# Optimization experiments

Measured on AMD Instinct MI355X. Metric: run time of the kernel, lower is better.

Reference implementation:

```python
import jax, jax.numpy as jnp
import numpy as np

SEQ_LEN = 2048
N_FFT = 4096   # rfft length n >= seq_len (repo uses next power of two of ~2*seq)
K = 24         # num_eigh
D = 768        # n_embd
BATCH = 1


def _spectral_filters(seq_len: int, k: int) -> jnp.ndarray:
    # Hankel matrix Z[i,j] = 2 / ((i+j)^3 - (i+j)), 1-indexed
    e = np.arange(1, seq_len + 1, dtype=np.float64)
    ipj = e[:, None] + e[None, :]
    Z = 2.0 / (ipj ** 3 - ipj)
    sigma, phi = np.linalg.eigh(Z)
    sigma, phi = sigma[-k:], phi[:, -k:]
    phi = phi * sigma ** 0.25
    return jnp.asarray(phi, dtype=jnp.float32)  # (seq_len, K)


def setup_inputs() -> dict:
    key = jax.random.key(0)
    k1, k2, k3 = jax.random.split(key, 3)
    x = jax.random.normal(k1, (BATCH, SEQ_LEN, D), dtype=jnp.float32)
    M_phi_plus = jax.random.normal(k2, (K, D, D), dtype=jnp.float32) * 0.02
    M_phi_minus = jax.random.normal(k3, (K, D, D), dtype=jnp.float32) * 0.02
    phi = _spectral_filters(SEQ_LEN, K)
    return {"x": x, "phi": phi, "M_phi_plus": M_phi_plus, "M_phi_minus": M_phi_minus}


def _convolve(u, v, n):
    # u: (b, seq, d), v: (seq, K)
    bsz, seq, d = u.shape
    k = v.shape[1]
    # alternating sign sequence (+1, -1, +1, ...)
    sgn = jnp.where(jnp.arange(seq) % 2 == 1, -1.0, 1.0)[None, :, None, None]  # (1,seq,1,1)
    V = jnp.fft.rfft(v.reshape(1, seq, k, 1, 1).astype(jnp.float32), n=n, axis=1)
    u4 = jnp.broadcast_to(u[:, :, None, :], (bsz, seq, k, d))  # (b,seq,K,d)
    U = jnp.stack([u4, u4 * sgn], axis=-1).astype(jnp.float32)  # (b,seq,K,d,2)
    Uf = jnp.fft.rfft(U, n=n, axis=1)
    U_conv = jnp.fft.irfft(V * Uf, n=n, axis=1)[:, :seq]  # (b,seq,K,d,2)
    U_plus = U_conv[..., 0]
    U_minus = U_conv[..., 1] * sgn
    return U_plus, U_minus


def reference(x, phi, M_phi_plus, M_phi_minus):
    U_plus, U_minus = _convolve(x, phi, N_FFT)
    spectral_plus = jnp.einsum('bskd,kde->bse', U_plus, M_phi_plus)
    spectral_minus = jnp.einsum('bskd,kde->bse', U_minus, M_phi_minus)
    return spectral_plus + spectral_minus
```

## Files before the change

### kernel.cpp

```cpp
#include <hip/hip_runtime.h>
#include <hip/hip_bf16.h>
#include <stdint.h>

#define SEQ 2048
#define DDIM 768
#define KF 24
#define NKV 48
#define NZC 8

typedef unsigned short ushort_t;
typedef __attribute__((ext_vector_type(8))) short short8;
typedef __attribute__((ext_vector_type(4))) float f32x4;

typedef __attribute__((address_space(3))) uint32_t lds_u32;
typedef __attribute__((address_space(1))) uint32_t glb_u32;

__device__ __forceinline__ unsigned short f2bf(float f) {
    union { float f; uint32_t u; } v; v.f = f;
    uint32_t u = v.u;
    return (unsigned short)((u + 0x7fff + ((u >> 16) & 1)) >> 16);
}


__global__ void k_pack_x(const float* __restrict__ x, ushort_t* __restrict__ xpk) {
    int b = blockIdx.x;
    int tt = b / 12, ks = b % 12;
    int tid = threadIdx.x;
    ushort_t* dst = xpk + (size_t)b * 8192;
    const float* src = x + (size_t)tt * 128 * DDIM + ks * 64;
#pragma unroll
    for (int p = 0; p < 4; ++p) {
        int s = p * 256 + tid;
        int row = s >> 3, sl = s & 7;
        const float* rp = src + (size_t)row * DDIM + sl * 8;
        float4 a = *(const float4*)rp;
        float4 c = *(const float4*)(rp + 4);
        ushort_t v[8] = {f2bf(a.x), f2bf(a.y), f2bf(a.z), f2bf(a.w),
                         f2bf(c.x), f2bf(c.y), f2bf(c.z), f2bf(c.w)};
        *(uint4*)(dst + row * 64 + ((sl ^ (row & 7)) << 3)) = *(uint4*)v;
    }
}

__global__ void k_pack_M(const float* __restrict__ Mp, const float* __restrict__ Mm,
                         ushort_t* __restrict__ Mpk) {
    __shared__ ushort_t lt[128 * 66];
    int b = blockIdx.x;
    int kv = b / 72; int rem = b % 72; int et = rem / 12, ks = rem % 12;
    const float* src = ((kv < KF) ? Mp + (size_t)kv * DDIM * DDIM
                                  : Mm + (size_t)(kv - KF) * DDIM * DDIM)
                       + (size_t)(ks * 64) * DDIM + et * 128;
    int tid = threadIdx.x;
#pragma unroll
    for (int p = 0; p < 32; ++p) {
        int lin = p * 256 + tid;
        int d = lin >> 7, e = lin & 127;
        lt[e * 66 + d] = f2bf(src[(size_t)d * DDIM + e]);
    }
    __syncthreads();
    ushort_t* dst = Mpk + (size_t)b * 8192;
#pragma unroll
    for (int p = 0; p < 4; ++p) {
        int s = p * 256 + tid; int row = s >> 3, sl = s & 7;
        ushort_t v[8];
#pragma unroll
        for (int j = 0; j < 8; ++j) v[j] = lt[row * 66 + sl * 8 + j];
        *(uint4*)(dst + row * 64 + ((sl ^ (row & 7)) << 3)) = *(uint4*)v;
    }
}

__global__ void k_build_T(const float* __restrict__ phi, ushort_t* __restrict__ Tpk) {
    __shared__ float phiL[256];
    int b = blockIdx.x;
    int kv = b / 17, slot = b % 17;
    int dm = slot - 1;
    int k = kv % KF; bool neg = kv >= KF;
    int tid = threadIdx.x;
    int tau = 128 * dm - 127 + tid;
    float v = 0.f;
    if (tid < 255 && tau >= 0 && tau < SEQ) {
        v = phi[(size_t)tau * KF + k];
        if (neg && (tau & 1)) v = -v;
    }
    phiL[tid] = v;
    __syncthreads();
    ushort_t* dst = Tpk + (size_t)b * 2 * 8192;
#pragma unroll
    for (int h = 0; h < 2; ++h) {
#pragma unroll
        for (int p = 0; p < 4; ++p) {
            int s = p * 256 + tid; int row = s >> 3, sl = s & 7;
            ushort_t v8[8];
#pragma unroll
            for (int j = 0; j < 8; ++j) {
                int col = h * 64 + sl * 8 + j;
                v8[j] = f2bf(phiL[row - col + 127]);
            }
            *(uint4*)(dst + h * 8192 + row * 64 + ((sl ^ (row & 7)) << 3)) = *(uint4*)v8;
        }
    }
}


__device__ __forceinline__ void read_frags(const ushort_t* As, const ushort_t* Bs,
                                           int lane, int wm, int wn, int kk,
                                           short8 av[4], short8 bv[4]) {
    int slot = kk * 4 + (lane >> 4);
#pragma unroll
    for (int m = 0; m < 4; ++m) {
        int row = wm * 64 + m * 16 + (lane & 15);
        av[m] = *(const short8*)(As + row * 64 + ((slot ^ (row & 7)) << 3));
    }
#pragma unroll
    for (int n = 0; n < 4; ++n) {
        int row = wn * 64 + n * 16 + (lane & 15);
        bv[n] = *(const short8*)(Bs + row * 64 + ((slot ^ (row & 7)) << 3));
    }
}

__device__ __forceinline__ void mfma16(const short8 av[4], const short8 bv[4], f32x4 acc[4][4]) {
    __builtin_amdgcn_s_setprio(1);
#pragma unroll
    for (int m = 0; m < 4; ++m)
#pragma unroll
        for (int n = 0; n < 4; ++n)
            acc[m][n] = __builtin_amdgcn_mfma_f32_16x16x32_bf16(av[m], bv[n], acc[m][n], 0, 0, 0);
    __builtin_amdgcn_s_setprio(0);
}

__global__ __launch_bounds__(256, 2)
void k_gemm_A(const ushort_t* __restrict__ Mpk, const ushort_t* __restrict__ xpk,
              ushort_t* __restrict__ Apk) {
    __shared__ ushort_t smem[2][2][8192];
    int bid = blockIdx.x;
    int lid = (bid & 7) * 576 + (bid >> 3);
    int kv = lid / 96; int rem = lid % 96; int et = rem / 16, tt = rem % 16;
    const ushort_t* Abase = Mpk + ((size_t)(kv * 6 + et) * 12) * 8192;
    const ushort_t* Bbase = xpk + (size_t)(tt * 12) * 8192;
    int tid = threadIdx.x, lane = tid & 63, wave = tid >> 6;
    int wm = wave >> 1, wn = wave & 1;

    auto stage4 = [&](const ushort_t* src, ushort_t* dst) {
        const char* s = (const char*)src + wave * 4096 + lane * 16;
        char* l = (char*)dst + wave * 4096;
#pragma unroll
        for (int p = 0; p < 4; ++p)
            __builtin_amdgcn_global_load_lds((const glb_u32*)(s + p * 1024),
                                             (lds_u32*)(l + p * 1024), 16, 0, 0);
    };

    f32x4 acc[4][4];
#pragma unroll
    for (int m = 0; m < 4; ++m)
#pragma unroll
        for (int n = 0; n < 4; ++n) acc[m][n] = (f32x4){0.f, 0.f, 0.f, 0.f};

    stage4(Abase, smem[0][0]);
    stage4(Bbase, smem[0][1]);

    for (int s = 0; s < 12; ++s) {
        int c = s & 1;
        bool more = (s + 1 < 12);
        if (more) {
            stage4(Abase + (s + 1) * 8192, smem[c ^ 1][0]);
            asm volatile("s_waitcnt vmcnt(4)" ::: "memory");
        } else {
            asm volatile("s_waitcnt vmcnt(0)" ::: "memory");
        }
        __builtin_amdgcn_s_barrier();
        __builtin_amdgcn_sched_barrier(0);

        const ushort_t* As = smem[c][0];
        const ushort_t* Bs = smem[c][1];
        short8 av[2][4], bv[2][4];
#pragma unroll
        for (int kk = 0; kk < 2; ++kk) {
            int slot = kk * 4 + (lane >> 4);
#pragma unroll
            for (int m = 0; m < 4; ++m) {
                int row = wm * 64 + m * 16 + (lane & 15);
                av[kk][m] = *(const short8*)(As + row * 64 + ((slot ^ (row & 7)) << 3));
            }
#pragma unroll
            for (int n = 0; n < 4; ++n) {
                int row = wn * 64 + n * 16 + (lane & 15);
                bv[kk][n] = *(const short8*)(Bs + row * 64 + ((slot ^ (row & 7)) << 3));
            }
        }
        if (more) stage4(Bbase + (s + 1) * 8192, smem[c ^ 1][1]);

        asm volatile("s_waitcnt lgkmcnt(0)" ::: "memory");
        __builtin_amdgcn_sched_barrier(0);

        __builtin_amdgcn_s_setprio(1);
#pragma unroll
        for (int kk = 0; kk < 2; ++kk)
#pragma unroll
            for (int m = 0; m < 4; ++m)
#pragma unroll
                for (int n = 0; n < 4; ++n)
                    acc[m][n] = __builtin_amdgcn_mfma_f32_16x16x32_bf16(av[kk][m], bv[kk][n], acc[m][n], 0, 0, 0);
        __builtin_amdgcn_s_setprio(0);
        __builtin_amdgcn_s_barrier();
    }

    ushort_t* sm = &smem[0][0][0];
#pragma unroll
    for (int m = 0; m < 4; ++m) {
        int rb = wm * 64 + m * 16 + ((lane >> 4) << 2);
#pragma unroll
        for (int n = 0; n < 4; ++n) {
            int cb = wn * 64 + n * 16 + (lane & 15);
            int h = cb >> 6, c6 = cb & 63, sl = c6 >> 3, j = c6 & 7;
#pragma unroll
            for (int r = 0; r < 4; ++r) {
                int row = rb + r;
                sm[h * 8192 + row * 64 + ((sl ^ (row & 7)) << 3) + j] = f2bf(acc[m][n][r]);
            }
        }
    }
    __syncthreads();
    uint4* d4 = (uint4*)(Apk + ((size_t)((kv * 6 + et) * 16 + tt) * 2) * 8192);
    const uint4* s4 = (const uint4*)sm;
#pragma unroll
    for (int p = 0; p < 8; ++p) d4[p * 256 + tid] = s4[p * 256 + tid];
}

__global__ __launch_bounds__(256, 2)
void k_gemm_Bv4(const ushort_t* __restrict__ Tpk, const ushort_t* __restrict__ Apk,
                float* __restrict__ outz) {
    __shared__ ushort_t smem[2][2][8192];

    int bid = blockIdx.x;
    int lid = (bid & 7) * 54 + (bid >> 3);
    int et = lid / 72;
    int cidx = lid % 72;
    int i1 = 0, zc = 0, base = 0;
#pragma unroll
    for (int t = 0; t < 16; ++t) {
        int cand = 15 - t;
        int nc = (cand >> 1) + 1;
        if (cidx < base + nc) { i1 = cand; zc = cidx - base; break; }
        base += nc;
    }
    int jlo = zc * 2;
    const int NS = NKV * 2 * 2;

    int tid = threadIdx.x, lane = tid & 63, wave = tid >> 6;
    int wm = wave >> 1, wn = wave & 1;

    f32x4 acc[4][4];
#pragma unroll
    for (int m = 0; m < 4; ++m)
#pragma unroll
        for (int n = 0; n < 4; ++n) acc[m][n] = (f32x4){0.f, 0.f, 0.f, 0.f};

    auto timg = [&](int kv, int jj, int h) -> const ushort_t* {
        return Tpk + ((size_t)((kv * 17 + (i1 - jj + 1)) * 2 + h)) * 8192;
    };
    auto aimg = [&](int kv, int jj, int h) -> const ushort_t* {
        return Apk + ((size_t)(((kv * 6 + et) * 16 + jj) * 2 + h)) * 8192;
    };
    auto stage4 = [&](const ushort_t* src, ushort_t* dst) {
        const char* s = (const char*)src + wave * 4096 + lane * 16;
        char* l = (char*)dst + wave * 4096;
#pragma unroll
        for (int p = 0; p < 4; ++p)
            __builtin_amdgcn_global_load_lds((const glb_u32*)(s + p * 1024),
                                             (lds_u32*)(l + p * 1024), 16, 0, 0);
    };

    int kv = 0, jj = jlo, h = 0;
    stage4(timg(kv, jj, h), smem[0][0]);
    stage4(aimg(kv, jj, h), smem[0][1]);

    for (int s = 0; s < NS; ++s) {
        int c = s & 1;
        int nh = h ^ 1, njj = jj, nkvv = kv;
        if (!nh) { njj = jj + 1; if (njj > jlo + 1) { njj = jlo; nkvv = kv + 1; } }
        bool more = (s + 1 < NS);

        if (more) {
            stage4(timg(nkvv, njj, nh), smem[c ^ 1][0]);
            asm volatile("s_waitcnt vmcnt(4)" ::: "memory");
        } else {
            asm volatile("s_waitcnt vmcnt(0)" ::: "memory");
        }
        __builtin_amdgcn_s_barrier();
        __builtin_amdgcn_sched_barrier(0);

        const ushort_t* As = smem[c][0];
        const ushort_t* Bs = smem[c][1];
        short8 av[2][4], bv[2][4];
#pragma unroll
        for (int kk = 0; kk < 2; ++kk) {
            int slot = kk * 4 + (lane >> 4);
#pragma unroll
            for (int m = 0; m < 4; ++m) {
                int row = wm * 64 + m * 16 + (lane & 15);
                av[kk][m] = *(const short8*)(As + row * 64 + ((slot ^ (row & 7)) << 3));
            }
#pragma unroll
            for (int n = 0; n < 4; ++n) {
                int row = wn * 64 + n * 16 + (lane & 15);
                bv[kk][n] = *(const short8*)(Bs + row * 64 + ((slot ^ (row & 7)) << 3));
            }
        }
        if (more) stage4(aimg(nkvv, njj, nh), smem[c ^ 1][1]);

        asm volatile("s_waitcnt lgkmcnt(0)" ::: "memory");
        __builtin_amdgcn_sched_barrier(0);

        __builtin_amdgcn_s_setprio(1);
#pragma unroll
        for (int kk = 0; kk < 2; ++kk)
#pragma unroll
            for (int m = 0; m < 4; ++m)
#pragma unroll
                for (int n = 0; n < 4; ++n)
                    acc[m][n] = __builtin_amdgcn_mfma_f32_16x16x32_bf16(av[kk][m], bv[kk][n], acc[m][n], 0, 0, 0);
        __builtin_amdgcn_s_setprio(0);
        __builtin_amdgcn_s_barrier();
        kv = nkvv; jj = njj; h = nh;
    }

    float* dst = outz + ((size_t)zc * SEQ + (size_t)i1 * 128) * DDIM + et * 128;
#pragma unroll
    for (int m = 0; m < 4; ++m) {
        int rb = wm * 64 + m * 16 + ((lane >> 4) << 2);
#pragma unroll
        for (int n = 0; n < 4; ++n) {
            int cb = wn * 64 + n * 16 + (lane & 15);
#pragma unroll
            for (int r = 0; r < 4; ++r)
                dst[(size_t)(rb + r) * DDIM + cb] = acc[m][n][r];
        }
    }
}

__global__ void k_reduce(const float* __restrict__ outz, float* __restrict__ out, int n4) {
    int idx = blockIdx.x * blockDim.x + threadIdx.x;
    if (idx < n4) {
        int srow = idx / (DDIM / 4);
        int zmax = srow >> 8;
        if (zmax > NZC - 1) zmax = NZC - 1;
        float4 s = ((const float4*)outz)[idx];
        for (int z = 1; z <= zmax; ++z) {
            float4 t = ((const float4*)(outz + (size_t)z * SEQ * DDIM))[idx];
            s.x += t.x; s.y += t.y; s.z += t.z; s.w += t.w;
        }
        ((float4*)out)[idx] = s;
    }
}

extern "C" void kernel_launch(void* const* d_in, const int* in_sizes, int n_in,
                              void* d_out, int out_size, void* d_ws, size_t ws_size,
                              hipStream_t stream) {
    (void)in_sizes; (void)n_in;
    const float* x   = (const float*)d_in[0];
    const float* phi = (const float*)d_in[1];
    const float* Mp  = (const float*)d_in[2];
    const float* Mm  = (const float*)d_in[3];
    float* out = (float*)d_out;

    char* ws = (char*)d_ws;
    size_t off = 0;
    auto alloc = [&](size_t bytes) { size_t o = off; off += (bytes + 255) & ~(size_t)255; return o; };
    size_t o_xpk = alloc((size_t)16 * 12 * 8192 * 2);
    size_t o_Mpk = alloc((size_t)NKV * 6 * 12 * 8192 * 2);
    size_t o_Tpk = alloc((size_t)NKV * 17 * 2 * 8192 * 2);
    size_t o_Apk = alloc((size_t)NKV * 6 * 16 * 2 * 8192 * 2);
    if (off > ws_size) {
        hipMemsetAsync(d_out, 0, (size_t)out_size * 4, stream);
        return;
    }

    ushort_t* xpk = (ushort_t*)(ws + o_xpk);
    ushort_t* Mpk = (ushort_t*)(ws + o_Mpk);
    ushort_t* Tpk = (ushort_t*)(ws + o_Tpk);
    ushort_t* Apk = (ushort_t*)(ws + o_Apk);
    float*   outz = (float*)(ws + o_Mpk);

    k_pack_x<<<16 * 12, 256, 0, stream>>>(x, xpk);
    k_pack_M<<<NKV * 6 * 12, 256, 0, stream>>>(Mp, Mm, Mpk);
    k_build_T<<<NKV * 17, 256, 0, stream>>>(phi, Tpk);
    k_gemm_A<<<NKV * 96, 256, 0, stream>>>(Mpk, xpk, Apk);
    k_gemm_Bv4<<<432, 256, 0, stream>>>(Tpk, Apk, outz);
    int n4 = SEQ * DDIM / 4;
    k_reduce<<<(n4 + 255) / 256, 256, 0, stream>>>(outz, out, n4);
}
```

Measured before the change: 325.1 us.

## Share one Toeplitz filter set between plus and minus branches via sign folding

The alternating-sign Toeplitz matrices for the minus branch are no longer built. One sign factor is folded into the gemm_A epilogue, by negating odd columns of the minus-branch A tiles. The other is applied at the end of the second GEMM, which keeps separate plus and minus accumulators and combines them with a row-parity sign. This halves the T build work and the T workspace footprint, and should improve cache reuse of T tiles. In exchange the second GEMM doubles its accumulator registers, which raises register pressure under the two-blocks-per-CU launch bound.

```diff
diff --git a/kernel.cpp b/kernel.cpp
--- a/kernel.cpp
+++ b/kernel.cpp
@@ -73,14 +73,11 @@
     int b = blockIdx.x;
     int kv = b / 17, slot = b % 17;
     int dm = slot - 1;
-    int k = kv % KF; bool neg = kv >= KF;
     int tid = threadIdx.x;
     int tau = 128 * dm - 127 + tid;
     float v = 0.f;
-    if (tid < 255 && tau >= 0 && tau < SEQ) {
-        v = phi[(size_t)tau * KF + k];
-        if (neg && (tau & 1)) v = -v;
-    }
+    if (tid < 255 && tau >= 0 && tau < SEQ)
+        v = phi[(size_t)tau * KF + kv];
     phiL[tid] = v;
     __syncthreads();
     ushort_t* dst = Tpk + (size_t)b * 2 * 8192;
@@ -203,6 +200,7 @@
         __builtin_amdgcn_s_barrier();
     }
 
+    float fs = (kv >= KF && (lane & 1)) ? -1.f : 1.f;
     ushort_t* sm = &smem[0][0][0];
 #pragma unroll
     for (int m = 0; m < 4; ++m) {
@@ -214,7 +212,7 @@
 #pragma unroll
             for (int r = 0; r < 4; ++r) {
                 int row = rb + r;
-                sm[h * 8192 + row * 64 + ((sl ^ (row & 7)) << 3) + j] = f2bf(acc[m][n][r]);
+                sm[h * 8192 + row * 64 + ((sl ^ (row & 7)) << 3) + j] = f2bf(fs * acc[m][n][r]);
             }
         }
     }
@@ -226,39 +224,37 @@
 }
 
 __global__ __launch_bounds__(256, 2)
-void k_gemm_Bv4(const ushort_t* __restrict__ Tpk, const ushort_t* __restrict__ Apk,
+void k_gemm_Bv6(const ushort_t* __restrict__ Tpk, const ushort_t* __restrict__ Apk,
                 float* __restrict__ outz) {
     __shared__ ushort_t smem[2][2][8192];
 
     int bid = blockIdx.x;
     int lid = (bid & 7) * 54 + (bid >> 3);
     int et = lid / 72;
-    int cidx = lid % 72;
-    int i1 = 0, zc = 0, base = 0;
-#pragma unroll
-    for (int t = 0; t < 16; ++t) {
-        int cand = 15 - t;
-        int nc = (cand >> 1) + 1;
-        if (cidx < base + nc) { i1 = cand; zc = cidx - base; break; }
-        base += nc;
-    }
+    int r = lid % 72;
+    int zc = 0;
+#pragma unroll
+    for (int z = 1; z < 8; ++z) if (r >= z * (17 - z)) zc = z;
+    int i1 = 2 * zc + (r - zc * (17 - zc));
     int jlo = zc * 2;
-    const int NS = NKV * 2 * 2;
 
     int tid = threadIdx.x, lane = tid & 63, wave = tid >> 6;
     int wm = wave >> 1, wn = wave & 1;
 
-    f32x4 acc[4][4];
+    f32x4 accp[4][4], accm[4][4];
 #pragma unroll
     for (int m = 0; m < 4; ++m)
 #pragma unroll
-        for (int n = 0; n < 4; ++n) acc[m][n] = (f32x4){0.f, 0.f, 0.f, 0.f};
-
-    auto timg = [&](int kv, int jj, int h) -> const ushort_t* {
-        return Tpk + ((size_t)((kv * 17 + (i1 - jj + 1)) * 2 + h)) * 8192;
+        for (int n = 0; n < 4; ++n) {
+            accp[m][n] = (f32x4){0.f, 0.f, 0.f, 0.f};
+            accm[m][n] = (f32x4){0.f, 0.f, 0.f, 0.f};
+        }
+
+    auto timg = [&](int kv24, int jjs, int h) -> const ushort_t* {
+        return Tpk + ((size_t)((kv24 * 17 + (i1 - (jlo + jjs) + 1)) * 2 + h)) * 8192;
     };
-    auto aimg = [&](int kv, int jj, int h) -> const ushort_t* {
-        return Apk + ((size_t)(((kv * 6 + et) * 16 + jj) * 2 + h)) * 8192;
+    auto aimg = [&](int kv24, int sign, int jjs, int h) -> const ushort_t* {
+        return Apk + ((size_t)((((kv24 + KF * sign) * 6 + et) * 16 + (jlo + jjs)) * 2 + h)) * 8192;
     };
     auto stage4 = [&](const ushort_t* src, ushort_t* dst) {
         const char* s = (const char*)src + wave * 4096 + lane * 16;
@@ -269,58 +265,71 @@
                                              (lds_u32*)(l + p * 1024), 16, 0, 0);
     };
 
-    int kv = 0, jj = jlo, h = 0;
-    stage4(timg(kv, jj, h), smem[0][0]);
-    stage4(aimg(kv, jj, h), smem[0][1]);
-
-    for (int s = 0; s < NS; ++s) {
-        int c = s & 1;
-        int nh = h ^ 1, njj = jj, nkvv = kv;
-        if (!nh) { njj = jj + 1; if (njj > jlo + 1) { njj = jlo; nkvv = kv + 1; } }
-        bool more = (s + 1 < NS);
-
-        if (more) {
-            stage4(timg(nkvv, njj, nh), smem[c ^ 1][0]);
-            asm volatile("s_waitcnt vmcnt(4)" ::: "memory");
-        } else {
-            asm volatile("s_waitcnt vmcnt(0)" ::: "memory");
-        }
-        __builtin_amdgcn_s_barrier();
-        __builtin_amdgcn_sched_barrier(0);
-
-        const ushort_t* As = smem[c][0];
-        const ushort_t* Bs = smem[c][1];
-        short8 av[2][4], bv[2][4];
-#pragma unroll
-        for (int kk = 0; kk < 2; ++kk) {
-            int slot = kk * 4 + (lane >> 4);
-#pragma unroll
-            for (int m = 0; m < 4; ++m) {
-                int row = wm * 64 + m * 16 + (lane & 15);
-                av[kk][m] = *(const short8*)(As + row * 64 + ((slot ^ (row & 7)) << 3));
-            }
-#pragma unroll
-            for (int n = 0; n < 4; ++n) {
-                int row = wn * 64 + n * 16 + (lane & 15);
-                bv[kk][n] = *(const short8*)(Bs + row * 64 + ((slot ^ (row & 7)) << 3));
-            }
-        }
-        if (more) stage4(aimg(nkvv, njj, nh), smem[c ^ 1][1]);
-
-        asm volatile("s_waitcnt lgkmcnt(0)" ::: "memory");
-        __builtin_amdgcn_sched_barrier(0);
-
-        __builtin_amdgcn_s_setprio(1);
-#pragma unroll
-        for (int kk = 0; kk < 2; ++kk)
-#pragma unroll
-            for (int m = 0; m < 4; ++m)
-#pragma unroll
-                for (int n = 0; n < 4; ++n)
-                    acc[m][n] = __builtin_amdgcn_mfma_f32_16x16x32_bf16(av[kk][m], bv[kk][n], acc[m][n], 0, 0, 0);
-        __builtin_amdgcn_s_setprio(0);
-        __builtin_amdgcn_s_barrier();
-        kv = nkvv; jj = njj; h = nh;
+    stage4(timg(0, 0, 0), smem[0][0]);
+    stage4(aimg(0, 0, 0, 0), smem[0][1]);
+
+    for (int kv24 = 0; kv24 < KF; ++kv24) {
+#pragma unroll
+        for (int rem = 0; rem < 8; ++rem) {
+            const int sign = (rem >> 1) & 1, h = rem & 1;
+            const int c = h;
+            const int nrem = (rem + 1) & 7;
+            const int njjs = nrem >> 2, nsign = (nrem >> 1) & 1, nh = nrem & 1;
+            int nkv = kv24 + (rem == 7);
+            bool more = (nkv < KF);
+
+            if (more) {
+                stage4(timg(nkv, njjs, nh), smem[c ^ 1][0]);
+                asm volatile("s_waitcnt vmcnt(4)" ::: "memory");
+            } else {
+                asm volatile("s_waitcnt vmcnt(0)" ::: "memory");
+            }
+            __builtin_amdgcn_s_barrier();
+            __builtin_amdgcn_sched_barrier(0);
+
+            const ushort_t* As = smem[c][0];
+            const ushort_t* Bs = smem[c][1];
+            short8 av[2][4], bv[2][4];
+#pragma unroll
+            for (int kk = 0; kk < 2; ++kk) {
+                int slot = kk * 4 + (lane >> 4);
+#pragma unroll
+                for (int m = 0; m < 4; ++m) {
+                    int row = wm * 64 + m * 16 + (lane & 15);
+                    av[kk][m] = *(const short8*)(As + row * 64 + ((slot ^ (row & 7)) << 3));
+                }
+#pragma unroll
+                for (int n = 0; n < 4; ++n) {
+                    int row = wn * 64 + n * 16 + (lane & 15);
+                    bv[kk][n] = *(const short8*)(Bs + row * 64 + ((slot ^ (row & 7)) << 3));
+                }
+            }
+            if (more) stage4(aimg(nkv, nsign, njjs, nh), smem[c ^ 1][1]);
+
+            asm volatile("s_waitcnt lgkmcnt(0)" ::: "memory");
+            __builtin_amdgcn_sched_barrier(0);
+
+            __builtin_amdgcn_s_setprio(1);
+            if (sign == 0) {
+#pragma unroll
+                for (int kk = 0; kk < 2; ++kk)
+#pragma unroll
+                    for (int m = 0; m < 4; ++m)
+#pragma unroll
+                        for (int n = 0; n < 4; ++n)
+                            accp[m][n] = __builtin_amdgcn_mfma_f32_16x16x32_bf16(av[kk][m], bv[kk][n], accp[m][n], 0, 0, 0);
+            } else {
+#pragma unroll
+                for (int kk = 0; kk < 2; ++kk)
+#pragma unroll
+                    for (int m = 0; m < 4; ++m)
+#pragma unroll
+                        for (int n = 0; n < 4; ++n)
+                            accm[m][n] = __builtin_amdgcn_mfma_f32_16x16x32_bf16(av[kk][m], bv[kk][n], accm[m][n], 0, 0, 0);
+            }
+            __builtin_amdgcn_s_setprio(0);
+            __builtin_amdgcn_s_barrier();
+        }
     }
 
     float* dst = outz + ((size_t)zc * SEQ + (size_t)i1 * 128) * DDIM + et * 128;
@@ -331,8 +340,11 @@
         for (int n = 0; n < 4; ++n) {
             int cb = wn * 64 + n * 16 + (lane & 15);
 #pragma unroll
-            for (int r = 0; r < 4; ++r)
-                dst[(size_t)(rb + r) * DDIM + cb] = acc[m][n][r];
+            for (int r4 = 0; r4 < 4; ++r4) {
+                float vm = accm[m][n][r4];
+                float v = accp[m][n][r4] + ((r4 & 1) ? -vm : vm);
+                dst[(size_t)(rb + r4) * DDIM + cb] = v;
+            }
         }
     }
 }
@@ -367,7 +379,7 @@
     auto alloc = [&](size_t bytes) { size_t o = off; off += (bytes + 255) & ~(size_t)255; return o; };
     size_t o_xpk = alloc((size_t)16 * 12 * 8192 * 2);
     size_t o_Mpk = alloc((size_t)NKV * 6 * 12 * 8192 * 2);
-    size_t o_Tpk = alloc((size_t)NKV * 17 * 2 * 8192 * 2);
+    size_t o_Tpk = alloc((size_t)KF * 17 * 2 * 8192 * 2);
     size_t o_Apk = alloc((size_t)NKV * 6 * 16 * 2 * 8192 * 2);
     if (off > ws_size) {
         hipMemsetAsync(d_out, 0, (size_t)out_size * 4, stream);
@@ -382,9 +394,9 @@
 
     k_pack_x<<<16 * 12, 256, 0, stream>>>(x, xpk);
     k_pack_M<<<NKV * 6 * 12, 256, 0, stream>>>(Mp, Mm, Mpk);
-    k_build_T<<<NKV * 17, 256, 0, stream>>>(phi, Tpk);
+    k_build_T<<<KF * 17, 256, 0, stream>>>(phi, Tpk);
     k_gemm_A<<<NKV * 96, 256, 0, stream>>>(Mpk, xpk, Apk);
-    k_gemm_Bv4<<<432, 256, 0, stream>>>(Tpk, Apk, outz);
+    k_gemm_Bv6<<<432, 256, 0, stream>>>(Tpk, Apk, outz);
     int n4 = SEQ * DDIM / 4;
     k_reduce<<<(n4 + 255) / 256, 256, 0, stream>>>(outz, out, n4);
 }
```

New measurement: 309.8 us. 4.7% less time.
